# Performance work log

Measured on AMD Instinct MI355X. Metric: run time of the kernel, lower is better.

The kernel has to match this reference:

```python
import jax, jax.numpy as jnp
import numpy as np

H = 256          # hidden_dim
NH = 4           # num_heads
HD = H // NH     # head_dim = 64
EPS = 1e-5


def _ln(x, g, b):
    m = jnp.mean(x, axis=-1, keepdims=True)
    v = jnp.mean(jnp.square(x - m), axis=-1, keepdims=True)
    return (x - m) * jax.lax.rsqrt(v + EPS) * g + b


def _mha1(q_in, kv_in, in_proj_w, in_proj_b, out_w, out_b):
    # Single-query / single-key multihead attention (seq_len == 1 on both sides).
    # q_in, kv_in: [B, H]
    Wq, Wk, Wv = jnp.split(in_proj_w, 3, axis=0)   # each [H, H]
    bq, bk, bv = jnp.split(in_proj_b, 3, axis=0)
    B = q_in.shape[0]
    q = (q_in @ Wq.T + bq).reshape(B, NH, HD)
    k = (kv_in @ Wk.T + bk).reshape(B, NH, HD)
    v = (kv_in @ Wv.T + bv).reshape(B, NH, HD)
    scores = jnp.sum(q * k, axis=-1, keepdims=True) / jnp.sqrt(jnp.float32(HD))  # [B,NH,1]
    w = jax.nn.softmax(scores, axis=-1)  # softmax over 1 key -> all ones
    out = (w * v).reshape(B, H)
    return out @ out_w.T + out_b


def setup_inputs() -> dict:
    key = jax.random.key(0)
    ks = jax.random.split(key, 16)
    B, BIO, TXT, NC = 65536, 32, 768, 2
    s = lambda n: 1.0 / np.sqrt(n)
    return {
        "bio": jax.random.normal(ks[0], (B, BIO), jnp.float32),
        "text": jax.random.normal(ks[1], (B, TXT), jnp.float32),
        "bio_w": jax.random.normal(ks[2], (H, BIO), jnp.float32) * s(BIO),
        "bio_b": jnp.zeros((H,), jnp.float32),
        "text_w": jax.random.normal(ks[3], (H, TXT), jnp.float32) * s(TXT),
        "text_b": jnp.zeros((H,), jnp.float32),
        "ln_bio_g": jnp.ones((H,), jnp.float32),
        "ln_bio_b": jnp.zeros((H,), jnp.float32),
        "ln_text_g": jnp.ones((H,), jnp.float32),
        "ln_text_b": jnp.zeros((H,), jnp.float32),
        "in_proj_w": jax.random.normal(ks[4], (3 * H, H), jnp.float32) * s(H),
        "in_proj_b": jnp.zeros((3 * H,), jnp.float32),
        "out_w": jax.random.normal(ks[5], (H, H), jnp.float32) * s(H),
        "out_b": jnp.zeros((H,), jnp.float32),
        "cls1_w": jax.random.normal(ks[6], (H, 2 * H), jnp.float32) * s(2 * H),
        "cls1_b": jnp.zeros((H,), jnp.float32),
        "cls_ln_g": jnp.ones((H,), jnp.float32),
        "cls_ln_b": jnp.zeros((H,), jnp.float32),
        "cls2_w": jax.random.normal(ks[7], (NC, H), jnp.float32) * s(H),
        "cls2_b": jnp.zeros((NC,), jnp.float32),
    }


def reference(bio, text, bio_w, bio_b, text_w, text_b, ln_bio_g, ln_bio_b,
              ln_text_g, ln_text_b, in_proj_w, in_proj_b, out_w, out_b,
              cls1_w, cls1_b, cls_ln_g, cls_ln_b, cls2_w, cls2_b):
    b = _ln(bio @ bio_w.T + bio_b, ln_bio_g, ln_bio_b)      # [B, H]
    t = _ln(text @ text_w.T + text_b, ln_text_g, ln_text_b)  # [B, H]
    attn_bio = _mha1(b, t, in_proj_w, in_proj_b, out_w, out_b)
    attn_text = _mha1(t, b, in_proj_w, in_proj_b, out_w, out_b)
    fused = jnp.concatenate([attn_bio, attn_text], axis=-1)  # [B, 2H]
    h = jax.nn.relu(_ln(fused @ cls1_w.T + cls1_b, cls_ln_g, cls_ln_b))
    return h @ cls2_w.T + cls2_b
```

## Files before the change

kernel.cpp:

```cpp
#include <hip/hip_runtime.h>

typedef __attribute__((ext_vector_type(4))) float f4;
typedef __attribute__((ext_vector_type(8))) short s8;

#define EPS 1e-5f

__device__ __forceinline__ unsigned short f2bf(float f) {
    union { float f; unsigned u; } v; v.f = f;
    unsigned u = v.u;
    return (unsigned short)((u + 0x7fffu + ((u >> 16) & 1u)) >> 16);
}
__device__ __forceinline__ unsigned pack2(float a, float b) {
    return (unsigned)f2bf(a) | ((unsigned)f2bf(b) << 16);
}
__device__ __forceinline__ s8 pack8(f4 a, f4 b) {
    union { s8 v; unsigned u[4]; } r;
    r.u[0] = pack2(a[0], a[1]); r.u[1] = pack2(a[2], a[3]);
    r.u[2] = pack2(b[0], b[1]); r.u[3] = pack2(b[2], b[3]);
    return r.v;
}

__global__ __launch_bounds__(256) void k_prep1(const float* __restrict__ text_w,
                                               const float* __restrict__ bio_w,
                                               const float* __restrict__ out_w,
                                               const float* __restrict__ in_proj_w,
                                               const float* __restrict__ in_proj_b,
                                               const float* __restrict__ out_b,
                                               unsigned short* __restrict__ twFL,
                                               unsigned short* __restrict__ bwFL,
                                               float* __restrict__ A,
                                               float* __restrict__ cvec) {
    int b = blockIdx.x, t = threadIdx.x;
    if (b < 96) {
        int idx = b * 256 + t;
        int ksg = idx >> 10;
        int rem = idx & 1023;
        int ct = rem >> 6, lane = rem & 63;
        int n  = ct * 16 + (lane & 15);
        int k0 = ksg * 32 + ((lane >> 4) << 3);
        const float* src = &text_w[n * 768 + k0];
        f4 a = *(const f4*)src, c = *(const f4*)(src + 4);
        unsigned* dst = (unsigned*)&twFL[idx * 8];
        dst[0] = pack2(a[0], a[1]); dst[1] = pack2(a[2], a[3]);
        dst[2] = pack2(c[0], c[1]); dst[3] = pack2(c[2], c[3]);
    } else if (b < 100) {
        int idx = (b - 96) * 256 + t;
        int ct = idx >> 6, lane = idx & 63;
        int n  = ct * 16 + (lane & 15);
        int k0 = (lane >> 4) << 3;
        const float* src = &bio_w[n * 32 + k0];
        f4 a = *(const f4*)src, c = *(const f4*)(src + 4);
        unsigned* dst = (unsigned*)&bwFL[idx * 8];
        dst[0] = pack2(a[0], a[1]); dst[1] = pack2(a[2], a[3]);
        dst[2] = pack2(c[0], c[1]); dst[3] = pack2(c[2], c[3]);
    } else {
        __shared__ float srow[256];
        __shared__ float red[256];
        int i = b - 100, j = t;
        srow[j] = out_w[i * 256 + j];
        __syncthreads();
        float acc = 0.f;
#pragma unroll 16
        for (int k = 0; k < 256; k++)
            acc = fmaf(srow[k], in_proj_w[(512 + k) * 256 + j], acc);
        A[i * 256 + j] = acc;
        red[j] = srow[j] * in_proj_b[512 + j];
        __syncthreads();
        for (int s = 128; s > 0; s >>= 1) {
            if (j < s) red[j] += red[j + s];
            __syncthreads();
        }
        if (j == 0) cvec[i] = red[0] + out_b[i];
    }
}

__global__ __launch_bounds__(256) void k_prep_PQ(const float* __restrict__ cls1_w,
                                                 const float* __restrict__ cls1_b,
                                                 const float* __restrict__ A,
                                                 const float* __restrict__ cvec,
                                                 const float* __restrict__ ln_text_g,
                                                 const float* __restrict__ ln_text_b,
                                                 const float* __restrict__ ln_bio_g,
                                                 const float* __restrict__ ln_bio_b,
                                                 unsigned short* __restrict__ pqFL,
                                                 float* __restrict__ dvec) {
    __shared__ float w1[256], w2[256], red[256];
    int i = blockIdx.x, j = threadIdx.x;
    w1[j] = cls1_w[i * 512 + j];
    w2[j] = cls1_w[i * 512 + 256 + j];
    __syncthreads();
    float rp = 0.f, rq = 0.f;
#pragma unroll 8
    for (int k = 0; k < 256; k++) {
        float a = A[k * 256 + j];
        rp = fmaf(w1[k], a, rp);
        rq = fmaf(w2[k], a, rq);
    }
    int ct   = i >> 4;
    int lane = (i & 15) | (((j >> 3) & 3) << 4);
    int jj   = j & 7;
    int ks1  = j >> 5;
    pqFL[(((ks1     ) * 16 + ct) * 64 + lane) * 8 + jj] = f2bf(rp * ln_text_g[j]);
    pqFL[(((ks1 + 8 ) * 16 + ct) * 64 + lane) * 8 + jj] = f2bf(rq * ln_bio_g[j]);
    red[j] = rp * ln_text_b[j] + rq * ln_bio_b[j] + (w1[j] + w2[j]) * cvec[j];
    __syncthreads();
    for (int s = 128; s > 0; s >>= 1) {
        if (j < s) red[j] += red[j + s];
        __syncthreads();
    }
    if (j == 0) dvec[i] = red[0] + cls1_b[i];
}

__global__ __launch_bounds__(512, 4) void k_main(
    const float* __restrict__ bio, const float* __restrict__ text,
    const float* __restrict__ bio_b, const float* __restrict__ text_b,
    const float* __restrict__ cls_ln_g, const float* __restrict__ cls_ln_b,
    const float* __restrict__ cls2_w, const float* __restrict__ cls2_b,
    const unsigned short* __restrict__ twFL, const unsigned short* __restrict__ bwFL,
    const unsigned short* __restrict__ pqFL, const float* __restrict__ dvec,
    float* __restrict__ out)
{
    __shared__ __align__(16) unsigned short s_n[64][520];
    __shared__ float s_red[4][64][2];

    const int tid  = threadIdx.x;
    const int wv   = tid >> 6;
    const int cs   = wv & 3;
    const int rh   = wv >> 2;
    const int lane = tid & 63;
    const int q    = lane >> 4;
    const int lr   = lane & 15;
    const int R0   = blockIdx.x * 64;

    f4 acc[2][4];
    float s1[2][4], s2[2][4], m_[2][4], iv_[2][4];

    {
        f4 bioA[2], bioB[2];
#pragma unroll
        for (int rt = 0; rt < 2; rt++) {
            const float* p = &bio[(size_t)(R0 + rh * 32 + rt * 16 + lr) * 32 + q * 8];
            bioA[rt] = *(const f4*)p;
            bioB[rt] = *(const f4*)(p + 4);
        }
        s8 bfrb[4];
#pragma unroll
        for (int c = 0; c < 4; c++)
            bfrb[c] = *(const s8*)&bwFL[((cs * 4 + c) * 64 + lane) * 8];
#pragma unroll
        for (int rt = 0; rt < 2; rt++)
#pragma unroll
            for (int c = 0; c < 4; c++) acc[rt][c] = (f4){0.f, 0.f, 0.f, 0.f};
#pragma unroll
        for (int rt = 0; rt < 2; rt++) {
            s8 af = pack8(bioA[rt], bioB[rt]);
#pragma unroll
            for (int c = 0; c < 4; c++)
                acc[rt][c] = __builtin_amdgcn_mfma_f32_16x16x32_bf16(af, bfrb[c], acc[rt][c], 0, 0, 0);
        }
    }
#pragma unroll
    for (int rt = 0; rt < 2; rt++)
#pragma unroll
        for (int r = 0; r < 4; r++) { s1[rt][r] = 0.f; s2[rt][r] = 0.f; }
#pragma unroll
    for (int rt = 0; rt < 2; rt++)
#pragma unroll
        for (int c = 0; c < 4; c++) {
            float bb = bio_b[cs * 64 + c * 16 + lr];
#pragma unroll
            for (int r = 0; r < 4; r++) {
                float x = acc[rt][c][r] + bb;
                acc[rt][c][r] = x;
                s1[rt][r] += x; s2[rt][r] += x * x;
            }
        }
#pragma unroll
    for (int off = 1; off < 16; off <<= 1)
#pragma unroll
        for (int rt = 0; rt < 2; rt++)
#pragma unroll
            for (int r = 0; r < 4; r++) {
                s1[rt][r] += __shfl_xor(s1[rt][r], off, 64);
                s2[rt][r] += __shfl_xor(s2[rt][r], off, 64);
            }
    if (lr == 0)
#pragma unroll
        for (int rt = 0; rt < 2; rt++)
#pragma unroll
            for (int r = 0; r < 4; r++) {
                int row = rh * 32 + rt * 16 + q * 4 + r;
                s_red[cs][row][0] = s1[rt][r];
                s_red[cs][row][1] = s2[rt][r];
            }
    __syncthreads();
#pragma unroll
    for (int rt = 0; rt < 2; rt++)
#pragma unroll
        for (int r = 0; r < 4; r++) {
            int row = rh * 32 + rt * 16 + q * 4 + r;
            float t1 = s_red[0][row][0] + s_red[1][row][0] + s_red[2][row][0] + s_red[3][row][0];
            float t2 = s_red[0][row][1] + s_red[1][row][1] + s_red[2][row][1] + s_red[3][row][1];
            float mm = t1 * (1.f / 256.f);
            float vv = t2 * (1.f / 256.f) - mm * mm;
            m_[rt][r]  = mm;
            iv_[rt][r] = rsqrtf(vv + EPS);
        }
#pragma unroll
    for (int rt = 0; rt < 2; rt++)
#pragma unroll
        for (int c = 0; c < 4; c++) {
            int col = cs * 64 + c * 16 + lr;
#pragma unroll
            for (int r = 0; r < 4; r++)
                s_n[rh * 32 + rt * 16 + q * 4 + r][256 + col] =
                    f2bf((acc[rt][c][r] - m_[rt][r]) * iv_[rt][r]);
        }

#pragma unroll
    for (int rt = 0; rt < 2; rt++)
#pragma unroll
        for (int c = 0; c < 4; c++) acc[rt][c] = (f4){0.f, 0.f, 0.f, 0.f};
    {
        const float* tb0 = &text[(size_t)(R0 + rh * 32 + lr) * 768 + q * 8];
        const float* tb1 = tb0 + 16 * 768;
        f4 a0lo = *(const f4*)tb0, a0hi = *(const f4*)(tb0 + 4);
        f4 a1lo = *(const f4*)tb1, a1hi = *(const f4*)(tb1 + 4);
        for (int ks = 0; ks < 24; ks++) {
            f4 n0lo, n0hi, n1lo, n1hi;
            if (ks < 23) {
                const float* p0 = tb0 + (ks + 1) * 32;
                const float* p1 = tb1 + (ks + 1) * 32;
                n0lo = *(const f4*)p0; n0hi = *(const f4*)(p0 + 4);
                n1lo = *(const f4*)p1; n1hi = *(const f4*)(p1 + 4);
            }
            s8 bfr[4];
#pragma unroll
            for (int c = 0; c < 4; c++)
                bfr[c] = *(const s8*)&twFL[((ks * 16 + cs * 4 + c) * 64 + lane) * 8];
            {
                s8 af0 = pack8(a0lo, a0hi);
                s8 af1 = pack8(a1lo, a1hi);
#pragma unroll
                for (int c = 0; c < 4; c++) {
                    acc[0][c] = __builtin_amdgcn_mfma_f32_16x16x32_bf16(af0, bfr[c], acc[0][c], 0, 0, 0);
                    acc[1][c] = __builtin_amdgcn_mfma_f32_16x16x32_bf16(af1, bfr[c], acc[1][c], 0, 0, 0);
                }
            }
            a0lo = n0lo; a0hi = n0hi; a1lo = n1lo; a1hi = n1hi;
        }
    }
#pragma unroll
    for (int rt = 0; rt < 2; rt++)
#pragma unroll
        for (int r = 0; r < 4; r++) { s1[rt][r] = 0.f; s2[rt][r] = 0.f; }
#pragma unroll
    for (int rt = 0; rt < 2; rt++)
#pragma unroll
        for (int c = 0; c < 4; c++) {
            float bb = text_b[cs * 64 + c * 16 + lr];
#pragma unroll
            for (int r = 0; r < 4; r++) {
                float x = acc[rt][c][r] + bb;
                acc[rt][c][r] = x;
                s1[rt][r] += x; s2[rt][r] += x * x;
            }
        }
#pragma unroll
    for (int off = 1; off < 16; off <<= 1)
#pragma unroll
        for (int rt = 0; rt < 2; rt++)
#pragma unroll
            for (int r = 0; r < 4; r++) {
                s1[rt][r] += __shfl_xor(s1[rt][r], off, 64);
                s2[rt][r] += __shfl_xor(s2[rt][r], off, 64);
            }
    __syncthreads();
    if (lr == 0)
#pragma unroll
        for (int rt = 0; rt < 2; rt++)
#pragma unroll
            for (int r = 0; r < 4; r++) {
                int row = rh * 32 + rt * 16 + q * 4 + r;
                s_red[cs][row][0] = s1[rt][r];
                s_red[cs][row][1] = s2[rt][r];
            }
    __syncthreads();
#pragma unroll
    for (int rt = 0; rt < 2; rt++)
#pragma unroll
        for (int r = 0; r < 4; r++) {
            int row = rh * 32 + rt * 16 + q * 4 + r;
            float t1 = s_red[0][row][0] + s_red[1][row][0] + s_red[2][row][0] + s_red[3][row][0];
            float t2 = s_red[0][row][1] + s_red[1][row][1] + s_red[2][row][1] + s_red[3][row][1];
            float mm = t1 * (1.f / 256.f);
            float vv = t2 * (1.f / 256.f) - mm * mm;
            m_[rt][r]  = mm;
            iv_[rt][r] = rsqrtf(vv + EPS);
        }
#pragma unroll
    for (int rt = 0; rt < 2; rt++)
#pragma unroll
        for (int c = 0; c < 4; c++) {
            int col = cs * 64 + c * 16 + lr;
#pragma unroll
            for (int r = 0; r < 4; r++)
                s_n[rh * 32 + rt * 16 + q * 4 + r][col] =
                    f2bf((acc[rt][c][r] - m_[rt][r]) * iv_[rt][r]);
        }
    __syncthreads();

#pragma unroll
    for (int rt = 0; rt < 2; rt++)
#pragma unroll
        for (int c = 0; c < 4; c++) {
            float dv = dvec[cs * 64 + c * 16 + lr];
            acc[rt][c] = (f4){dv, dv, dv, dv};
        }
#pragma unroll 4
    for (int ks = 0; ks < 16; ks++) {
        s8 bfr[4];
#pragma unroll
        for (int c = 0; c < 4; c++)
            bfr[c] = *(const s8*)&pqFL[((ks * 16 + cs * 4 + c) * 64 + lane) * 8];
#pragma unroll
        for (int rt = 0; rt < 2; rt++) {
            s8 af = *(const s8*)&s_n[rh * 32 + rt * 16 + lr][ks * 32 + q * 8];
#pragma unroll
            for (int c = 0; c < 4; c++)
                acc[rt][c] = __builtin_amdgcn_mfma_f32_16x16x32_bf16(af, bfr[c], acc[rt][c], 0, 0, 0);
        }
    }

#pragma unroll
    for (int rt = 0; rt < 2; rt++)
#pragma unroll
        for (int r = 0; r < 4; r++) { s1[rt][r] = 0.f; s2[rt][r] = 0.f; }
#pragma unroll
    for (int rt = 0; rt < 2; rt++)
#pragma unroll
        for (int c = 0; c < 4; c++)
#pragma unroll
            for (int r = 0; r < 4; r++) {
                float x = acc[rt][c][r];
                s1[rt][r] += x; s2[rt][r] += x * x;
            }
#pragma unroll
    for (int off = 1; off < 16; off <<= 1)
#pragma unroll
        for (int rt = 0; rt < 2; rt++)
#pragma unroll
            for (int r = 0; r < 4; r++) {
                s1[rt][r] += __shfl_xor(s1[rt][r], off, 64);
                s2[rt][r] += __shfl_xor(s2[rt][r], off, 64);
            }
    __syncthreads();
    if (lr == 0)
#pragma unroll
        for (int rt = 0; rt < 2; rt++)
#pragma unroll
            for (int r = 0; r < 4; r++) {
                int row = rh * 32 + rt * 16 + q * 4 + r;
                s_red[cs][row][0] = s1[rt][r];
                s_red[cs][row][1] = s2[rt][r];
            }
    __syncthreads();
#pragma unroll
    for (int rt = 0; rt < 2; rt++)
#pragma unroll
        for (int r = 0; r < 4; r++) {
            int row = rh * 32 + rt * 16 + q * 4 + r;
            float t1 = s_red[0][row][0] + s_red[1][row][0] + s_red[2][row][0] + s_red[3][row][0];
            float t2 = s_red[0][row][1] + s_red[1][row][1] + s_red[2][row][1] + s_red[3][row][1];
            float mm = t1 * (1.f / 256.f);
            float vv = t2 * (1.f / 256.f) - mm * mm;
            m_[rt][r]  = mm;
            iv_[rt][r] = rsqrtf(vv + EPS);
        }
    float po0[2][4], po1[2][4];
#pragma unroll
    for (int rt = 0; rt < 2; rt++)
#pragma unroll
        for (int r = 0; r < 4; r++) { po0[rt][r] = 0.f; po1[rt][r] = 0.f; }
#pragma unroll
    for (int rt = 0; rt < 2; rt++)
#pragma unroll
        for (int c = 0; c < 4; c++) {
            int col = cs * 64 + c * 16 + lr;
            float gg = cls_ln_g[col], bb = cls_ln_b[col];
            float c0 = cls2_w[col],   c1 = cls2_w[256 + col];
#pragma unroll
            for (int r = 0; r < 4; r++) {
                float h = fmaxf((acc[rt][c][r] - m_[rt][r]) * iv_[rt][r] * gg + bb, 0.f);
                po0[rt][r] = fmaf(h, c0, po0[rt][r]);
                po1[rt][r] = fmaf(h, c1, po1[rt][r]);
            }
        }
#pragma unroll
    for (int off = 1; off < 16; off <<= 1)
#pragma unroll
        for (int rt = 0; rt < 2; rt++)
#pragma unroll
            for (int r = 0; r < 4; r++) {
                po0[rt][r] += __shfl_xor(po0[rt][r], off, 64);
                po1[rt][r] += __shfl_xor(po1[rt][r], off, 64);
            }
    __syncthreads();
    if (lr == 0)
#pragma unroll
        for (int rt = 0; rt < 2; rt++)
#pragma unroll
            for (int r = 0; r < 4; r++) {
                int row = rh * 32 + rt * 16 + q * 4 + r;
                s_red[cs][row][0] = po0[rt][r];
                s_red[cs][row][1] = po1[rt][r];
            }
    __syncthreads();
    if (tid < 128) {
        int row = tid >> 1, comp = tid & 1;
        float v = s_red[0][row][comp] + s_red[1][row][comp] +
                  s_red[2][row][comp] + s_red[3][row][comp];
        out[(size_t)(R0 + row) * 2 + comp] = v + cls2_b[comp];
    }
}

extern "C" void kernel_launch(void* const* d_in, const int* in_sizes, int n_in,
                              void* d_out, int out_size, void* d_ws, size_t ws_size,
                              hipStream_t stream) {
    const float* bio       = (const float*)d_in[0];
    const float* text      = (const float*)d_in[1];
    const float* bio_w     = (const float*)d_in[2];
    const float* bio_b     = (const float*)d_in[3];
    const float* text_w    = (const float*)d_in[4];
    const float* text_b    = (const float*)d_in[5];
    const float* ln_bio_g  = (const float*)d_in[6];
    const float* ln_bio_b  = (const float*)d_in[7];
    const float* ln_text_g = (const float*)d_in[8];
    const float* ln_text_b = (const float*)d_in[9];
    const float* in_proj_w = (const float*)d_in[10];
    const float* in_proj_b = (const float*)d_in[11];
    const float* out_w     = (const float*)d_in[12];
    const float* out_b     = (const float*)d_in[13];
    const float* cls1_w    = (const float*)d_in[14];
    const float* cls1_b    = (const float*)d_in[15];
    const float* cls_ln_g  = (const float*)d_in[16];
    const float* cls_ln_b  = (const float*)d_in[17];
    const float* cls2_w    = (const float*)d_in[18];
    const float* cls2_b    = (const float*)d_in[19];
    float* out = (float*)d_out;

    float* ws   = (float*)d_ws;
    float* A    = ws;
    float* cvec = ws + 65536;
    float* dvec = ws + 65792;
    unsigned short* us   = (unsigned short*)(ws + 66048);
    unsigned short* twFL = us;
    unsigned short* bwFL = us + 196608;
    unsigned short* pqFL = us + 204800;

    k_prep1  <<<356, 256, 0, stream>>>(text_w, bio_w, out_w, in_proj_w, in_proj_b, out_b,
                                       twFL, bwFL, A, cvec);
    k_prep_PQ<<<256, 256, 0, stream>>>(cls1_w, cls1_b, A, cvec,
                                       ln_text_g, ln_text_b, ln_bio_g, ln_bio_b,
                                       pqFL, dvec);

    int nrows = in_sizes[0] / 32;
    k_main<<<nrows / 64, 512, 0, stream>>>(bio, text, bio_b, text_b,
                                           cls_ln_g, cls_ln_b, cls2_w, cls2_b,
                                           twFL, bwFL, pqFL, dvec, out);
}
```

Baseline: 448.5 us.

## Split fused main kernel into normalize and classifier kernels via global bf16 buffer

Splits k_main into two kernels. k_N stages text tiles into shared memory as bf16 with coalesced loads and writes the normalized bio/text activations to a global bf16 workspace buffer. k_Z reads that buffer and runs the classifier GEMM, LayerNorm and final projection. Rows are processed in chunks sized to the available workspace. This cuts the large per-block shared array, which should raise occupancy and improve text-load coalescing, at the cost of a global round trip of 1 KB per row and an extra launch per chunk.

```diff
diff --git a/kernel.cpp b/kernel.cpp
--- a/kernel.cpp
+++ b/kernel.cpp
@@ -111,16 +111,13 @@
     if (j == 0) dvec[i] = red[0] + cls1_b[i];
 }
 
-__global__ __launch_bounds__(512, 4) void k_main(
+__global__ __launch_bounds__(512, 4) void k_N(
     const float* __restrict__ bio, const float* __restrict__ text,
     const float* __restrict__ bio_b, const float* __restrict__ text_b,
-    const float* __restrict__ cls_ln_g, const float* __restrict__ cls_ln_b,
-    const float* __restrict__ cls2_w, const float* __restrict__ cls2_b,
     const unsigned short* __restrict__ twFL, const unsigned short* __restrict__ bwFL,
-    const unsigned short* __restrict__ pqFL, const float* __restrict__ dvec,
-    float* __restrict__ out)
+    unsigned short* __restrict__ nbuf, int row0)
 {
-    __shared__ __align__(16) unsigned short s_n[64][520];
+    __shared__ __align__(16) unsigned short s_x[64][200];
     __shared__ float s_red[4][64][2];
 
     const int tid  = threadIdx.x;
@@ -131,6 +128,7 @@
     const int q    = lane >> 4;
     const int lr   = lane & 15;
     const int R0   = blockIdx.x * 64;
+    const int GR0  = row0 + R0;
 
     f4 acc[2][4];
     float s1[2][4], s2[2][4], m_[2][4], iv_[2][4];
@@ -139,7 +137,7 @@
         f4 bioA[2], bioB[2];
 #pragma unroll
         for (int rt = 0; rt < 2; rt++) {
-            const float* p = &bio[(size_t)(R0 + rh * 32 + rt * 16 + lr) * 32 + q * 8];
+            const float* p = &bio[(size_t)(GR0 + rh * 32 + rt * 16 + lr) * 32 + q * 8];
             bioA[rt] = *(const f4*)p;
             bioB[rt] = *(const f4*)(p + 4);
         }
@@ -210,10 +208,10 @@
     for (int rt = 0; rt < 2; rt++)
 #pragma unroll
         for (int c = 0; c < 4; c++) {
-            int col = cs * 64 + c * 16 + lr;
+            int col = 256 + cs * 64 + c * 16 + lr;
 #pragma unroll
             for (int r = 0; r < 4; r++)
-                s_n[rh * 32 + rt * 16 + q * 4 + r][256 + col] =
+                nbuf[(size_t)(R0 + rh * 32 + rt * 16 + q * 4 + r) * 512 + col] =
                     f2bf((acc[rt][c][r] - m_[rt][r]) * iv_[rt][r]);
         }
 
@@ -221,33 +219,33 @@
     for (int rt = 0; rt < 2; rt++)
 #pragma unroll
         for (int c = 0; c < 4; c++) acc[rt][c] = (f4){0.f, 0.f, 0.f, 0.f};
-    {
-        const float* tb0 = &text[(size_t)(R0 + rh * 32 + lr) * 768 + q * 8];
-        const float* tb1 = tb0 + 16 * 768;
-        f4 a0lo = *(const f4*)tb0, a0hi = *(const f4*)(tb0 + 4);
-        f4 a1lo = *(const f4*)tb1, a1hi = *(const f4*)(tb1 + 4);
-        for (int ks = 0; ks < 24; ks++) {
-            f4 n0lo, n0hi, n1lo, n1hi;
-            if (ks < 23) {
-                const float* p0 = tb0 + (ks + 1) * 32;
-                const float* p1 = tb1 + (ks + 1) * 32;
-                n0lo = *(const f4*)p0; n0hi = *(const f4*)(p0 + 4);
-                n1lo = *(const f4*)p1; n1hi = *(const f4*)(p1 + 4);
-            }
+
+    for (int ch = 0; ch < 4; ch++) {
+        __syncthreads();
+#pragma unroll
+        for (int i = 0; i < 6; i++) {
+            int idx = tid + i * 512;
+            int row = idx / 48;
+            int c4  = idx - row * 48;
+            f4 v = *(const f4*)&text[(size_t)(GR0 + row) * 768 + ch * 192 + c4 * 4];
+            uint2 p; p.x = pack2(v[0], v[1]); p.y = pack2(v[2], v[3]);
+            *(uint2*)&s_x[row][c4 * 4] = p;
+        }
+        __syncthreads();
+        int ksg0 = ch * 6;
+#pragma unroll
+        for (int ks = 0; ks < 6; ks++) {
             s8 bfr[4];
 #pragma unroll
             for (int c = 0; c < 4; c++)
-                bfr[c] = *(const s8*)&twFL[((ks * 16 + cs * 4 + c) * 64 + lane) * 8];
-            {
-                s8 af0 = pack8(a0lo, a0hi);
-                s8 af1 = pack8(a1lo, a1hi);
-#pragma unroll
-                for (int c = 0; c < 4; c++) {
-                    acc[0][c] = __builtin_amdgcn_mfma_f32_16x16x32_bf16(af0, bfr[c], acc[0][c], 0, 0, 0);
-                    acc[1][c] = __builtin_amdgcn_mfma_f32_16x16x32_bf16(af1, bfr[c], acc[1][c], 0, 0, 0);
-                }
-            }
-            a0lo = n0lo; a0hi = n0hi; a1lo = n1lo; a1hi = n1hi;
+                bfr[c] = *(const s8*)&twFL[(((ksg0 + ks) * 16 + cs * 4 + c) * 64 + lane) * 8];
+#pragma unroll
+            for (int rt = 0; rt < 2; rt++) {
+                s8 af = *(const s8*)&s_x[rh * 32 + rt * 16 + lr][ks * 32 + q * 8];
+#pragma unroll
+                for (int c = 0; c < 4; c++)
+                    acc[rt][c] = __builtin_amdgcn_mfma_f32_16x16x32_bf16(af, bfr[c], acc[rt][c], 0, 0, 0);
+            }
         }
     }
 #pragma unroll
@@ -275,7 +273,6 @@
                 s1[rt][r] += __shfl_xor(s1[rt][r], off, 64);
                 s2[rt][r] += __shfl_xor(s2[rt][r], off, 64);
             }
-    __syncthreads();
     if (lr == 0)
 #pragma unroll
         for (int rt = 0; rt < 2; rt++)
@@ -305,10 +302,33 @@
             int col = cs * 64 + c * 16 + lr;
 #pragma unroll
             for (int r = 0; r < 4; r++)
-                s_n[rh * 32 + rt * 16 + q * 4 + r][col] =
+                nbuf[(size_t)(R0 + rh * 32 + rt * 16 + q * 4 + r) * 512 + col] =
                     f2bf((acc[rt][c][r] - m_[rt][r]) * iv_[rt][r]);
         }
-    __syncthreads();
+}
+
+__global__ __launch_bounds__(512, 4) void k_Z(
+    const unsigned short* __restrict__ nbuf,
+    const unsigned short* __restrict__ pqFL,
+    const float* __restrict__ dvec,
+    const float* __restrict__ cls_ln_g, const float* __restrict__ cls_ln_b,
+    const float* __restrict__ cls2_w, const float* __restrict__ cls2_b,
+    float* __restrict__ out, int row0)
+{
+    __shared__ float s_red[4][64][2];
+
+    const int tid  = threadIdx.x;
+    const int wv   = tid >> 6;
+    const int cs   = wv & 3;
+    const int rh   = wv >> 2;
+    const int lane = tid & 63;
+    const int q    = lane >> 4;
+    const int lr   = lane & 15;
+    const int R0   = blockIdx.x * 64;
+    const int GR0  = row0 + R0;
+
+    f4 acc[2][4];
+    float s1[2][4], s2[2][4], m_[2][4], iv_[2][4];
 
 #pragma unroll
     for (int rt = 0; rt < 2; rt++)
@@ -317,18 +337,19 @@
             float dv = dvec[cs * 64 + c * 16 + lr];
             acc[rt][c] = (f4){dv, dv, dv, dv};
         }
+    const unsigned short* nb0 = &nbuf[(size_t)(R0 + rh * 32 + lr) * 512 + q * 8];
 #pragma unroll 4
     for (int ks = 0; ks < 16; ks++) {
         s8 bfr[4];
 #pragma unroll
         for (int c = 0; c < 4; c++)
             bfr[c] = *(const s8*)&pqFL[((ks * 16 + cs * 4 + c) * 64 + lane) * 8];
-#pragma unroll
-        for (int rt = 0; rt < 2; rt++) {
-            s8 af = *(const s8*)&s_n[rh * 32 + rt * 16 + lr][ks * 32 + q * 8];
-#pragma unroll
-            for (int c = 0; c < 4; c++)
-                acc[rt][c] = __builtin_amdgcn_mfma_f32_16x16x32_bf16(af, bfr[c], acc[rt][c], 0, 0, 0);
+        s8 af0 = *(const s8*)&nb0[ks * 32];
+        s8 af1 = *(const s8*)&nb0[16 * 512 + ks * 32];
+#pragma unroll
+        for (int c = 0; c < 4; c++) {
+            acc[0][c] = __builtin_amdgcn_mfma_f32_16x16x32_bf16(af0, bfr[c], acc[0][c], 0, 0, 0);
+            acc[1][c] = __builtin_amdgcn_mfma_f32_16x16x32_bf16(af1, bfr[c], acc[1][c], 0, 0, 0);
         }
     }
 
@@ -354,7 +375,6 @@
                 s1[rt][r] += __shfl_xor(s1[rt][r], off, 64);
                 s2[rt][r] += __shfl_xor(s2[rt][r], off, 64);
             }
-    __syncthreads();
     if (lr == 0)
 #pragma unroll
         for (int rt = 0; rt < 2; rt++)
@@ -420,7 +440,7 @@
         int row = tid >> 1, comp = tid & 1;
         float v = s_red[0][row][comp] + s_red[1][row][comp] +
                   s_red[2][row][comp] + s_red[3][row][comp];
-        out[(size_t)(R0 + row) * 2 + comp] = v + cls2_b[comp];
+        out[(size_t)(GR0 + row) * 2 + comp] = v + cls2_b[comp];
     }
 }
 
@@ -457,6 +477,16 @@
     unsigned short* twFL = us;
     unsigned short* bwFL = us + 196608;
     unsigned short* pqFL = us + 204800;
+    unsigned short* nbuf = us + 335872;
+    size_t used_bytes = (size_t)66048 * 4 + (size_t)335872 * 2;
+
+    int nrows = in_sizes[0] / 32;
+
+    size_t avail = ws_size > used_bytes ? ws_size - used_bytes : 0;
+    long maxrows = (long)(avail / 1024);
+    int chunk = (int)((maxrows / 64) * 64);
+    if (chunk > nrows) chunk = nrows;
+    if (chunk < 64) chunk = 64;
 
     k_prep1  <<<356, 256, 0, stream>>>(text_w, bio_w, out_w, in_proj_w, in_proj_b, out_b,
                                        twFL, bwFL, A, cvec);
@@ -464,8 +494,12 @@
                                        ln_text_g, ln_text_b, ln_bio_g, ln_bio_b,
                                        pqFL, dvec);
 
-    int nrows = in_sizes[0] / 32;
-    k_main<<<nrows / 64, 512, 0, stream>>>(bio, text, bio_b, text_b,
+    for (int r0 = 0; r0 < nrows; r0 += chunk) {
+        int rows = nrows - r0 < chunk ? nrows - r0 : chunk;
+        k_N<<<rows / 64, 512, 0, stream>>>(bio, text, bio_b, text_b,
+                                           twFL, bwFL, nbuf, r0);
+        k_Z<<<rows / 64, 512, 0, stream>>>(nbuf, pqFL, dvec,
                                            cls_ln_g, cls_ln_b, cls2_w, cls2_b,
-                                           twFL, bwFL, pqFL, dvec, out);
-}
+                                           out, r0);
+    }
+}
```

After: 427.5 us. -4.7%, faster.
